# Performance work log

Hardware: AMD Instinct MI355X
Metric: run time of the kernel (lower is better)

The kernel has to match this reference:

```python
import jax, jax.numpy as jnp
import numpy as np

# static module config (matches init_kwargs)
DIM = 128
HEADS = 8
DW, HW, WW = 5, 7, 7  # depth/height/width window


def _neighbor_indices(D, H, W):
    """Flat circular-neighborhood indices, shape (P, n) with P=D*H*W, n=DW*HW*WW."""
    od = np.arange(DW) - (DW - 1) // 2
    oh = np.arange(HW) - (HW - 1) // 2
    ow = np.arange(WW) - (WW - 1) // 2
    dd = (np.arange(D)[:, None] + od[None, :]) % D   # (D, DW)
    hh = (np.arange(H)[:, None] + oh[None, :]) % H   # (H, HW)
    ww = (np.arange(W)[:, None] + ow[None, :]) % W   # (W, WW)
    idx = (dd[:, None, None, :, None, None] * (H * W)
           + hh[None, :, None, None, :, None] * W
           + ww[None, None, :, None, None, :])        # (D,H,W,DW,HW,WW)
    return jnp.asarray(idx.reshape(D * H * W, DW * HW * WW), dtype=jnp.int32)


def setup_inputs() -> dict:
    key = jax.random.key(0)
    k1, k2, k3, k4, k5 = jax.random.split(key, 5)
    B, D, H, W, C = 1, 5, 24, 48, DIM
    w_scale = 1.0 / np.sqrt(C)  # keep attention logits in a sane range
    return {
        "x": jax.random.normal(k1, (B, D, H, W, C), dtype=jnp.float32),
        "qkv_w": jax.random.normal(k2, (3 * C, C), dtype=jnp.float32) * w_scale,
        "qkv_b": jax.random.normal(k3, (3 * C,), dtype=jnp.float32) * 0.01,
        "proj_w": jax.random.normal(k4, (C, C), dtype=jnp.float32) * w_scale,
        "proj_b": jax.random.normal(k5, (C,), dtype=jnp.float32) * 0.01,
    }


def reference(x, qkv_w, qkv_b, proj_w, proj_b):
    B, D, H, W, C = x.shape
    P = D * H * W
    n = DW * HW * WW
    hd = C // HEADS
    scale = hd ** -0.5
    idx = _neighbor_indices(D, H, W)                      # (P, n) int32, static

    xf = x.reshape(B, P, C)
    qkv = xf @ qkv_w.T + qkv_b                            # (B, P, 3C)
    q, k, v = jnp.split(qkv, 3, axis=-1)

    q = q.reshape(B, P, HEADS, hd)                        # center-pixel query
    k_g = k[:, idx].reshape(B, P, n, HEADS, hd)           # gathered circular neighborhood
    v_g = v[:, idx].reshape(B, P, n, HEADS, hd)

    scores = jnp.einsum('bphd,bpnhd->bhpn', q, k_g) * scale
    attn = jax.nn.softmax(scores, axis=-1)                # softmax over 245 neighbors
    out = jnp.einsum('bhpn,bpnhd->bphd', attn, v_g).reshape(B, P, C)
    out = out @ proj_w.T + proj_b
    return out.reshape(B, D, H, W, C)
```

## Files before the change

kernel.cpp:

```cpp
#include <hip/hip_runtime.h>
#include <hip/hip_bf16.h>
#include <cstddef>

#define DIMC   128
#define NHEADS 8
#define HDIM   16
#define DD     5
#define HH     24
#define WW_    48
#define NPOS   (DD * HH * WW_)
#define SCALE  0.25f

typedef short  bf16x8 __attribute__((ext_vector_type(8)));
typedef float  f32x4  __attribute__((ext_vector_type(4)));

__device__ __forceinline__ unsigned short f2bf(float f) {
    unsigned u = __float_as_uint(f);
    u = (u + 0x7FFFu + ((u >> 16) & 1u)) >> 16;
    return (unsigned short)u;
}
__device__ __forceinline__ float bf2f(unsigned short s) {
    return __uint_as_float(((unsigned)s) << 16);
}

__global__ __launch_bounds__(256, 3) void gemm_qkv_kernel(
    const float* __restrict__ x,
    const float* __restrict__ wq,
    const float* __restrict__ qkv_b,
    unsigned short* __restrict__ Qhl,
    unsigned short* __restrict__ Kbf,
    unsigned short* __restrict__ Vbf)
{
    __shared__ __align__(16) unsigned short Bs[64][264];

    const int tid = threadIdx.x;
    const int bn  = blockIdx.x * 64;
    const int bm  = blockIdx.y * 64;

    for (int i = tid; i < 2048; i += 256) {
        const int r = i >> 5, c4 = (i & 31) * 4;
        const float4 v = *(const float4*)(wq + (size_t)(bn + r) * 128 + c4);
        ushort4 hi, lo;
        hi.x = f2bf(v.x); hi.y = f2bf(v.y); hi.z = f2bf(v.z); hi.w = f2bf(v.w);
        lo.x = f2bf(v.x - bf2f(hi.x));
        lo.y = f2bf(v.y - bf2f(hi.y));
        lo.z = f2bf(v.z - bf2f(hi.z));
        lo.w = f2bf(v.w - bf2f(hi.w));
        *(ushort4*)(&Bs[r][c4])       = hi;
        *(ushort4*)(&Bs[r][128 + c4]) = lo;
    }
    __syncthreads();

    const int w    = tid >> 6;
    const int lane = tid & 63;
    const int ln   = lane & 15;
    const int quad = lane >> 4;
    const int row  = bm + w * 16 + ln;
    const float* ar = x + (size_t)row * 128 + quad * 8;

    f32x4 acc[4] = {};
    #pragma unroll
    for (int kcg = 0; kcg < 4; ++kcg) {
        const float4 xa = *(const float4*)(ar + kcg * 32);
        const float4 xb = *(const float4*)(ar + kcg * 32 + 4);
        bf16x8 ahi, alo;
        {
            const float vv[8] = {xa.x, xa.y, xa.z, xa.w, xb.x, xb.y, xb.z, xb.w};
            #pragma unroll
            for (int j = 0; j < 8; ++j) {
                const unsigned short hh = f2bf(vv[j]);
                ahi[j] = (short)hh;
                alo[j] = (short)f2bf(vv[j] - bf2f(hh));
            }
        }
        #pragma unroll
        for (int nt = 0; nt < 4; ++nt) {
            const bf16x8 bhi = *(const bf16x8*)(&Bs[nt * 16 + ln][kcg * 32 + quad * 8]);
            const bf16x8 blo = *(const bf16x8*)(&Bs[nt * 16 + ln][128 + kcg * 32 + quad * 8]);
            acc[nt] = __builtin_amdgcn_mfma_f32_16x16x32_bf16(ahi, bhi, acc[nt], 0, 0, 0);
            acc[nt] = __builtin_amdgcn_mfma_f32_16x16x32_bf16(alo, bhi, acc[nt], 0, 0, 0);
            acc[nt] = __builtin_amdgcn_mfma_f32_16x16x32_bf16(ahi, blo, acc[nt], 0, 0, 0);
        }
    }

    #pragma unroll
    for (int nt = 0; nt < 4; ++nt) {
        const int col = bn + nt * 16 + ln;
        const float bv = qkv_b[col];
        #pragma unroll
        for (int r = 0; r < 4; ++r) {
            const int orow = bm + w * 16 + quad * 4 + r;
            const float val = acc[nt][r] + bv;
            if (col < 128) {
                const int h = col >> 4, ci = col & 15;
                const unsigned short hi = f2bf(val);
                Qhl[(size_t)orow * 256 + h * 32 + ci]      = hi;
                Qhl[(size_t)orow * 256 + h * 32 + 16 + ci] = f2bf(val - bf2f(hi));
            } else if (col < 256) {
                Kbf[(size_t)orow * 128 + (col - 128)] = f2bf(val);
            } else {
                Vbf[(size_t)orow * 128 + (col - 256)] = f2bf(val);
            }
        }
    }
}

__global__ __launch_bounds__(128, 2) void gemm_proj_kernel(
    const float* __restrict__ Opart,
    const float* __restrict__ Lpart,
    const float* __restrict__ wp,
    const float* __restrict__ proj_b,
    float* __restrict__ out)
{
    __shared__ __align__(16) unsigned short Bs[64][264];

    const int tid = threadIdx.x;
    const int bn  = blockIdx.x * 64;
    const int bm  = blockIdx.y * 32;

    for (int i = tid; i < 2048; i += 128) {
        const int r = i >> 5, c4 = (i & 31) * 4;
        const float4 v = *(const float4*)(wp + (size_t)(bn + r) * 128 + c4);
        ushort4 hi, lo;
        hi.x = f2bf(v.x); hi.y = f2bf(v.y); hi.z = f2bf(v.z); hi.w = f2bf(v.w);
        lo.x = f2bf(v.x - bf2f(hi.x));
        lo.y = f2bf(v.y - bf2f(hi.y));
        lo.z = f2bf(v.z - bf2f(hi.z));
        lo.w = f2bf(v.w - bf2f(hi.w));
        *(ushort4*)(&Bs[r][c4])       = hi;
        *(ushort4*)(&Bs[r][128 + c4]) = lo;
    }
    __syncthreads();

    const int w    = tid >> 6;
    const int lane = tid & 63;
    const int ln   = lane & 15;
    const int quad = lane >> 4;
    const int row  = bm + w * 16 + ln;

    float linv[8];
    {
        const float4 l0a = *(const float4*)(Lpart + (size_t)row * 8);
        const float4 l0b = *(const float4*)(Lpart + (size_t)row * 8 + 4);
        const float4 l1a = *(const float4*)(Lpart + (size_t)(NPOS + row) * 8);
        const float4 l1b = *(const float4*)(Lpart + (size_t)(NPOS + row) * 8 + 4);
        linv[0] = 1.0f / (l0a.x + l1a.x); linv[1] = 1.0f / (l0a.y + l1a.y);
        linv[2] = 1.0f / (l0a.z + l1a.z); linv[3] = 1.0f / (l0a.w + l1a.w);
        linv[4] = 1.0f / (l0b.x + l1b.x); linv[5] = 1.0f / (l0b.y + l1b.y);
        linv[6] = 1.0f / (l0b.z + l1b.z); linv[7] = 1.0f / (l0b.w + l1b.w);
    }
    const float* o0 = Opart + (size_t)row * 128 + quad * 8;
    const float* o1 = o0 + (size_t)NPOS * 128;

    f32x4 acc[4] = {};
    #pragma unroll
    for (int kcg = 0; kcg < 4; ++kcg) {
        const float4 a0 = *(const float4*)(o0 + kcg * 32);
        const float4 a0b = *(const float4*)(o0 + kcg * 32 + 4);
        const float4 a1 = *(const float4*)(o1 + kcg * 32);
        const float4 a1b = *(const float4*)(o1 + kcg * 32 + 4);
        const float inv = linv[kcg * 2 + (quad >> 1)];
        const float vv[8] = {
            (a0.x + a1.x) * inv, (a0.y + a1.y) * inv,
            (a0.z + a1.z) * inv, (a0.w + a1.w) * inv,
            (a0b.x + a1b.x) * inv, (a0b.y + a1b.y) * inv,
            (a0b.z + a1b.z) * inv, (a0b.w + a1b.w) * inv };
        bf16x8 ahi, alo;
        #pragma unroll
        for (int j = 0; j < 8; ++j) {
            const unsigned short hh = f2bf(vv[j]);
            ahi[j] = (short)hh;
            alo[j] = (short)f2bf(vv[j] - bf2f(hh));
        }
        #pragma unroll
        for (int nt = 0; nt < 4; ++nt) {
            const bf16x8 bhi = *(const bf16x8*)(&Bs[nt * 16 + ln][kcg * 32 + quad * 8]);
            const bf16x8 blo = *(const bf16x8*)(&Bs[nt * 16 + ln][128 + kcg * 32 + quad * 8]);
            acc[nt] = __builtin_amdgcn_mfma_f32_16x16x32_bf16(ahi, bhi, acc[nt], 0, 0, 0);
            acc[nt] = __builtin_amdgcn_mfma_f32_16x16x32_bf16(alo, bhi, acc[nt], 0, 0, 0);
            acc[nt] = __builtin_amdgcn_mfma_f32_16x16x32_bf16(ahi, blo, acc[nt], 0, 0, 0);
        }
    }

    #pragma unroll
    for (int nt = 0; nt < 4; ++nt) {
        const int col = bn + nt * 16 + ln;
        const float bv = proj_b[col];
        #pragma unroll
        for (int r = 0; r < 4; ++r) {
            const int orow = bm + w * 16 + quad * 4 + r;
            out[(size_t)orow * 128 + col] = acc[nt][r] + bv;
        }
    }
}

__global__ __launch_bounds__(256, 4) void attn_kernel(
    const unsigned short* __restrict__ Qhl,
    const unsigned short* __restrict__ Kbf,
    const unsigned short* __restrict__ Vbf,
    float* __restrict__ Opart,
    float* __restrict__ Lpart)
{
    __shared__ __align__(16) char smem[26368];
    unsigned short (*Vt)[264] = (unsigned short(*)[264])smem;
    unsigned short (*Qb)[40]  = (unsigned short(*)[40])(smem + 8448);
    unsigned short* PwBase    = (unsigned short*)(smem + 14848);
    float* red_l              = (float*)(smem + 25088);
    float* redO               = (float*)smem;

    const int bx   = blockIdx.x;
    const int tile = bx >> 1;
    const int half = bx & 1;
    const int h    = blockIdx.y;
    const int ty0  = (tile / 12) * 4;
    const int tx0  = (tile % 12) * 4;
    const int tid  = threadIdx.x;

    for (int i = tid; i < 512; i += 256) {
        const int ul = i >> 1, hf8 = i & 1;
        const int u  = half * 256 + ul;
        if (u < 500) {
            const int dp = u / 100;
            const int rr = u - dp * 100;
            const int yy = rr / 10;
            const int xx = rr - yy * 10;
            int y = ty0 - 3 + yy; if (y < 0) y += HH;  if (y >= HH) y -= HH;
            int x = tx0 - 3 + xx; if (x < 0) x += WW_; if (x >= WW_) x -= WW_;
            const int g = (dp * HH + y) * WW_ + x;
            const bf16x8 v = *(const bf16x8*)(Vbf + (size_t)g * 128 + h * 16 + hf8 * 8);
            #pragma unroll
            for (int c = 0; c < 8; ++c) Vt[hf8 * 8 + c][ul] = (unsigned short)v[c];
        } else {
            #pragma unroll
            for (int c = 0; c < 8; ++c) Vt[hf8 * 8 + c][ul] = 0;
        }
    }
    for (int i = tid; i < 320; i += 256) {
        const int p = i >> 2, seg = i & 3;
        const int d = p >> 4, s = p & 15;
        const int sy = s >> 2, sx = s & 3;
        const int g = (d * HH + ty0 + sy) * WW_ + tx0 + sx;
        *(bf16x8*)(&Qb[p][seg * 8]) = *(const bf16x8*)(Qhl + (size_t)g * 256 + h * 32 + seg * 8);
    }
    __syncthreads();

    const int w    = tid >> 6;
    const int lane = tid & 63;
    const int ln   = lane & 15;
    const int quad = lane >> 4;
    const int sy   = ln >> 2, sx = ln & 3;

    unsigned short* Pw = PwBase + w * 1280;

    bf16x8 qf[5];
    #pragma unroll
    for (int mt = 0; mt < 5; ++mt)
        qf[mt] = *(const bf16x8*)(&Qb[mt * 16 + ln][quad * 8]);

    f32x4 Ow[5] = {};
    float lsum[5] = {};

    #pragma unroll
    for (int chunk = 0; chunk < 2; ++chunk) {
        const int u0g = (half * 8 + w * 2 + chunk) * 32;
        const int u0l = (w * 2 + chunk) * 32;

        int rowa, rowb;
        {
            const int ua = u0g + ln      < 500 ? u0g + ln      : 499;
            const int ub = u0g + 16 + ln < 500 ? u0g + 16 + ln : 499;
            int dp = ua / 100, rr = ua - dp * 100, yy = rr / 10, xx = rr - yy * 10;
            int y = ty0 - 3 + yy; if (y < 0) y += HH;  if (y >= HH) y -= HH;
            int x = tx0 - 3 + xx; if (x < 0) x += WW_; if (x >= WW_) x -= WW_;
            rowa = (dp * HH + y) * WW_ + x;
            dp = ub / 100; rr = ub - dp * 100; yy = rr / 10; xx = rr - yy * 10;
            y = ty0 - 3 + yy; if (y < 0) y += HH;  if (y >= HH) y -= HH;
            x = tx0 - 3 + xx; if (x < 0) x += WW_; if (x >= WW_) x -= WW_;
            rowb = (dp * HH + y) * WW_ + x;
        }
        const bf16x8 ka = *(const bf16x8*)(Kbf + (size_t)rowa * 128 + h * 16 + (quad & 1) * 8);
        const bf16x8 kb = *(const bf16x8*)(Kbf + (size_t)rowb * 128 + h * 16 + (quad & 1) * 8);

        bool msk[2][4];
        #pragma unroll
        for (int b = 0; b < 2; ++b)
            #pragma unroll
            for (int r = 0; r < 4; ++r) {
                const int u = u0g + 16 * b + 4 * quad + r;
                const int rr = u % 100;
                const int uy = rr / 10, ux = rr - uy * 10;
                msk[b][r] = (u < 500) && ((unsigned)(uy - sy) <= 6u)
                                      && ((unsigned)(ux - sx) <= 6u);
            }

        const bf16x8 vf = *(const bf16x8*)(&Vt[ln][u0l + quad * 8]);

        #pragma unroll
        for (int mt = 0; mt < 5; ++mt) {
            f32x4 s0 = __builtin_amdgcn_mfma_f32_16x16x32_bf16(
                ka, qf[mt], (f32x4){0.f, 0.f, 0.f, 0.f}, 0, 0, 0);
            f32x4 s1 = __builtin_amdgcn_mfma_f32_16x16x32_bf16(
                kb, qf[mt], (f32x4){0.f, 0.f, 0.f, 0.f}, 0, 0, 0);

            unsigned short* pw = Pw + (mt & 1) * 640 + ln * 40;
            #pragma unroll
            for (int b = 0; b < 2; ++b) {
                const f32x4 s = b ? s1 : s0;
                unsigned short e[4];
                #pragma unroll
                for (int r = 0; r < 4; ++r) {
                    const float ev = msk[b][r] ? __expf(fmaf(s[r], SCALE, -8.0f)) : 0.f;
                    e[r] = f2bf(ev);
                    lsum[mt] += bf2f(e[r]);
                }
                *(unsigned*)(pw + 16 * b + 4 * quad)     = (unsigned)e[0] | ((unsigned)e[1] << 16);
                *(unsigned*)(pw + 16 * b + 4 * quad + 2) = (unsigned)e[2] | ((unsigned)e[3] << 16);
            }
            const bf16x8 pf = *(const bf16x8*)(Pw + (mt & 1) * 640 + ln * 40 + quad * 8);
            Ow[mt] = __builtin_amdgcn_mfma_f32_16x16x32_bf16(vf, pf, Ow[mt], 0, 0, 0);
        }
    }

    #pragma unroll
    for (int mt = 0; mt < 5; ++mt) {
        lsum[mt] += __shfl_xor(lsum[mt], 16);
        lsum[mt] += __shfl_xor(lsum[mt], 32);
    }

    __syncthreads();

    if (quad == 0) {
        #pragma unroll
        for (int mt = 0; mt < 5; ++mt)
            red_l[w * 80 + mt * 16 + ln] = lsum[mt];
    }
    #pragma unroll
    for (int mt = 0; mt < 5; ++mt)
        #pragma unroll
        for (int r = 0; r < 4; ++r)
            redO[(size_t)((w * 5 + mt) * 16 + quad * 4 + r) * 16 + ln] = Ow[mt][r];
    __syncthreads();

    for (int i = tid; i < 1280; i += 256) {
        const int m = i >> 4, c = i & 15;
        const int mt = m >> 4, mloc = m & 15;
        float o = 0.f, l = 0.f;
        #pragma unroll
        for (int w4 = 0; w4 < 4; ++w4) {
            o += redO[(size_t)((w4 * 5 + mt) * 16 + c) * 16 + mloc];
            l += red_l[w4 * 80 + m];
        }
        const int qsy = (mloc >> 2), qsx = mloc & 3;
        const size_t g = (size_t)((mt * HH + ty0 + qsy) * WW_ + (tx0 + qsx));
        Opart[((size_t)half * NPOS + g) * 128 + h * HDIM + c] = o;
        if (c == 0) Lpart[((size_t)half * NPOS + g) * 8 + h] = l;
    }
}

extern "C" void kernel_launch(void* const* d_in, const int* in_sizes, int n_in,
                              void* d_out, int out_size, void* d_ws, size_t ws_size,
                              hipStream_t stream)
{
    const float* x      = (const float*)d_in[0];
    const float* qkv_w  = (const float*)d_in[1];
    const float* qkv_b  = (const float*)d_in[2];
    const float* proj_w = (const float*)d_in[3];
    const float* proj_b = (const float*)d_in[4];
    float* out = (float*)d_out;

    char* ws = (char*)d_ws;
    unsigned short* Qhl   = (unsigned short*)ws;  ws += (size_t)NPOS * 256 * 2;
    unsigned short* Kbf   = (unsigned short*)ws;  ws += (size_t)NPOS * 128 * 2;
    unsigned short* Vbf   = (unsigned short*)ws;  ws += (size_t)NPOS * 128 * 2;
    float*          Opart = (float*)ws;           ws += (size_t)2 * NPOS * 128 * 4;
    float*          Lpart = (float*)ws;           ws += (size_t)2 * NPOS * 8 * 4;

    {
        dim3 grid(384 / 64, NPOS / 64);
        gemm_qkv_kernel<<<grid, 256, 0, stream>>>(x, qkv_w, qkv_b, Qhl, Kbf, Vbf);
    }
    {
        dim3 grid(144, NHEADS);
        attn_kernel<<<grid, 256, 0, stream>>>(Qhl, Kbf, Vbf, Opart, Lpart);
    }
    {
        dim3 grid(DIMC / 64, NPOS / 32);
        gemm_proj_kernel<<<grid, 128, 0, stream>>>(Opart, Lpart, proj_w, proj_b, out);
    }
}
```

Measured before the change: 98.86 us.

## Repartition attention work so each wave owns one depth slice, drop cross-wave reduction

The attention kernel now launches 5 waves per block, each handling one depth slice of 16 queries across all 256 keys, instead of 4 waves splitting keys across all 80 queries. This removes the shared-memory reduction of partial outputs and sums and the extra barriers, and lets each wave write its result directly with vector stores. Key row indices and neighbourhood masks are precomputed once into shared memory as an index table and bitmasks. Softmax probabilities are rearranged into the MFMA operand layout with cross-lane shuffles instead of a shared-memory round trip. In exchange, each wave now gathers K for every key chunk itself, which adds redundant global loads across waves.

```diff
diff --git a/kernel.cpp b/kernel.cpp
--- a/kernel.cpp
+++ b/kernel.cpp
@@ -194,19 +194,17 @@
     }
 }
 
-__global__ __launch_bounds__(256, 4) void attn_kernel(
+__global__ __launch_bounds__(320, 4) void attn_kernel(
     const unsigned short* __restrict__ Qhl,
     const unsigned short* __restrict__ Kbf,
     const unsigned short* __restrict__ Vbf,
     float* __restrict__ Opart,
     float* __restrict__ Lpart)
 {
-    __shared__ __align__(16) char smem[26368];
-    unsigned short (*Vt)[264] = (unsigned short(*)[264])smem;
-    unsigned short (*Qb)[40]  = (unsigned short(*)[40])(smem + 8448);
-    unsigned short* PwBase    = (unsigned short*)(smem + 14848);
-    float* red_l              = (float*)(smem + 25088);
-    float* redO               = (float*)smem;
+    __shared__ __align__(16) unsigned short Vt[16][258];
+    __shared__ __align__(16) unsigned short Qb[80][40];
+    __shared__ int RowL[256];
+    __shared__ unsigned short Mb[16][18];
 
     const int bx   = blockIdx.x;
     const int tile = bx >> 1;
@@ -216,16 +214,36 @@
     const int tx0  = (tile % 12) * 4;
     const int tid  = threadIdx.x;
 
-    for (int i = tid; i < 512; i += 256) {
+    for (int ul = tid; ul < 256; ul += 320) {
+        int u = half * 256 + ul; if (u > 499) u = 499;
+        const int dp = u / 100, rr = u % 100;
+        const int uy = rr / 10,  ux = rr % 10;
+        int y = ty0 - 3 + uy; if (y < 0) y += HH;  if (y >= HH) y -= HH;
+        int x = tx0 - 3 + ux; if (x < 0) x += WW_; if (x >= WW_) x -= WW_;
+        RowL[ul] = (dp * HH + y) * WW_ + x;
+    }
+    for (int i = tid; i < 256; i += 320) {
+        const int t = i >> 4, ql = i & 15;
+        const int qsy = ql >> 2, qsx = ql & 3;
+        unsigned bits = 0;
+        #pragma unroll
+        for (int b = 0; b < 16; ++b) {
+            const int u = half * 256 + t * 16 + b;
+            const int rr = u % 100;
+            const int uy = rr / 10, ux = rr % 10;
+            if (u < 500 && (unsigned)(uy - qsy) <= 6u && (unsigned)(ux - qsx) <= 6u)
+                bits |= 1u << b;
+        }
+        Mb[ql][t] = (unsigned short)bits;
+    }
+    for (int i = tid; i < 512; i += 320) {
         const int ul = i >> 1, hf8 = i & 1;
         const int u  = half * 256 + ul;
         if (u < 500) {
-            const int dp = u / 100;
-            const int rr = u - dp * 100;
-            const int yy = rr / 10;
-            const int xx = rr - yy * 10;
-            int y = ty0 - 3 + yy; if (y < 0) y += HH;  if (y >= HH) y -= HH;
-            int x = tx0 - 3 + xx; if (x < 0) x += WW_; if (x >= WW_) x -= WW_;
+            const int dp = u / 100, rr = u % 100;
+            const int uy = rr / 10,  ux = rr % 10;
+            int y = ty0 - 3 + uy; if (y < 0) y += HH;  if (y >= HH) y -= HH;
+            int x = tx0 - 3 + ux; if (x < 0) x += WW_; if (x >= WW_) x -= WW_;
             const int g = (dp * HH + y) * WW_ + x;
             const bf16x8 v = *(const bf16x8*)(Vbf + (size_t)g * 128 + h * 16 + hf8 * 8);
             #pragma unroll
@@ -235,11 +253,11 @@
             for (int c = 0; c < 8; ++c) Vt[hf8 * 8 + c][ul] = 0;
         }
     }
-    for (int i = tid; i < 320; i += 256) {
-        const int p = i >> 2, seg = i & 3;
+    {
+        const int p = tid >> 2, seg = tid & 3;
         const int d = p >> 4, s = p & 15;
-        const int sy = s >> 2, sx = s & 3;
-        const int g = (d * HH + ty0 + sy) * WW_ + tx0 + sx;
+        const int qsy = s >> 2, qsx = s & 3;
+        const int g = (d * HH + ty0 + qsy) * WW_ + tx0 + qsx;
         *(bf16x8*)(&Qb[p][seg * 8]) = *(const bf16x8*)(Qhl + (size_t)g * 256 + h * 32 + seg * 8);
     }
     __syncthreads();
@@ -248,113 +266,73 @@
     const int lane = tid & 63;
     const int ln   = lane & 15;
     const int quad = lane >> 4;
-    const int sy   = ln >> 2, sx = ln & 3;
-
-    unsigned short* Pw = PwBase + w * 1280;
-
-    bf16x8 qf[5];
-    #pragma unroll
-    for (int mt = 0; mt < 5; ++mt)
-        qf[mt] = *(const bf16x8*)(&Qb[mt * 16 + ln][quad * 8]);
-
-    f32x4 Ow[5] = {};
-    float lsum[5] = {};
-
-    #pragma unroll
-    for (int chunk = 0; chunk < 2; ++chunk) {
-        const int u0g = (half * 8 + w * 2 + chunk) * 32;
-        const int u0l = (w * 2 + chunk) * 32;
-
-        int rowa, rowb;
-        {
-            const int ua = u0g + ln      < 500 ? u0g + ln      : 499;
-            const int ub = u0g + 16 + ln < 500 ? u0g + 16 + ln : 499;
-            int dp = ua / 100, rr = ua - dp * 100, yy = rr / 10, xx = rr - yy * 10;
-            int y = ty0 - 3 + yy; if (y < 0) y += HH;  if (y >= HH) y -= HH;
-            int x = tx0 - 3 + xx; if (x < 0) x += WW_; if (x >= WW_) x -= WW_;
-            rowa = (dp * HH + y) * WW_ + x;
-            dp = ub / 100; rr = ub - dp * 100; yy = rr / 10; xx = rr - yy * 10;
-            y = ty0 - 3 + yy; if (y < 0) y += HH;  if (y >= HH) y -= HH;
-            x = tx0 - 3 + xx; if (x < 0) x += WW_; if (x >= WW_) x -= WW_;
-            rowb = (dp * HH + y) * WW_ + x;
-        }
-        const bf16x8 ka = *(const bf16x8*)(Kbf + (size_t)rowa * 128 + h * 16 + (quad & 1) * 8);
-        const bf16x8 kb = *(const bf16x8*)(Kbf + (size_t)rowb * 128 + h * 16 + (quad & 1) * 8);
-
-        bool msk[2][4];
-        #pragma unroll
-        for (int b = 0; b < 2; ++b)
-            #pragma unroll
-            for (int r = 0; r < 4; ++r) {
-                const int u = u0g + 16 * b + 4 * quad + r;
-                const int rr = u % 100;
-                const int uy = rr / 10, ux = rr - uy * 10;
-                msk[b][r] = (u < 500) && ((unsigned)(uy - sy) <= 6u)
-                                      && ((unsigned)(ux - sx) <= 6u);
-            }
+
+    const bf16x8 qf = *(const bf16x8*)(&Qb[w * 16 + ln][quad * 8]);
+    f32x4 Ow = {0.f, 0.f, 0.f, 0.f};
+    float lsum = 0.f;
+
+    const int koff = h * 16 + (quad & 1) * 8;
+    const int qa   = (quad & 1) << 1;
+    const int srcA = ln + (qa << 4);
+    const int srcB = srcA + 16;
+    const bool hi2 = quad >= 2;
+
+    #pragma unroll 2
+    for (int c = 0; c < 8; ++c) {
+        const int u0l = c * 32;
+        const int g0 = RowL[u0l + ln];
+        const int g1 = RowL[u0l + 16 + ln];
+        const bf16x8 ka = *(const bf16x8*)(Kbf + (size_t)g0 * 128 + koff);
+        const bf16x8 kb = *(const bf16x8*)(Kbf + (size_t)g1 * 128 + koff);
+        const unsigned mb = *(const unsigned*)(&Mb[ln][2 * c]);
+        const unsigned m0 = (mb >> (quad * 4)) & 0xF;
+        const unsigned m1 = (mb >> (16 + quad * 4)) & 0xF;
+
+        f32x4 s0 = __builtin_amdgcn_mfma_f32_16x16x32_bf16(ka, qf, (f32x4){0.f,0.f,0.f,0.f}, 0, 0, 0);
+        f32x4 s1 = __builtin_amdgcn_mfma_f32_16x16x32_bf16(kb, qf, (f32x4){0.f,0.f,0.f,0.f}, 0, 0, 0);
+
+        unsigned short e0[4], e1[4];
+        #pragma unroll
+        for (int r = 0; r < 4; ++r) {
+            const float v0 = ((m0 >> r) & 1u) ? __expf(fmaf(s0[r], SCALE, -8.0f)) : 0.f;
+            const float v1 = ((m1 >> r) & 1u) ? __expf(fmaf(s1[r], SCALE, -8.0f)) : 0.f;
+            e0[r] = f2bf(v0);
+            e1[r] = f2bf(v1);
+            lsum += bf2f(e0[r]) + bf2f(e1[r]);
+        }
+        const int dA = (int)((unsigned)e0[0] | ((unsigned)e0[1] << 16));
+        const int dB = (int)((unsigned)e0[2] | ((unsigned)e0[3] << 16));
+        const int dC = (int)((unsigned)e1[0] | ((unsigned)e1[1] << 16));
+        const int dD = (int)((unsigned)e1[2] | ((unsigned)e1[3] << 16));
+
+        const int xA = __shfl(dA, srcA, 64);
+        const int yC = __shfl(dC, srcA, 64);
+        const int xB = __shfl(dB, srcA, 64);
+        const int yD = __shfl(dD, srcA, 64);
+        const int zA = __shfl(dA, srcB, 64);
+        const int wC = __shfl(dC, srcB, 64);
+        const int zB = __shfl(dB, srcB, 64);
+        const int wD = __shfl(dD, srcB, 64);
+
+        union { int u[4]; bf16x8 v; } pf;
+        pf.u[0] = hi2 ? yC : xA;
+        pf.u[1] = hi2 ? yD : xB;
+        pf.u[2] = hi2 ? wC : zA;
+        pf.u[3] = hi2 ? wD : zB;
 
         const bf16x8 vf = *(const bf16x8*)(&Vt[ln][u0l + quad * 8]);
-
-        #pragma unroll
-        for (int mt = 0; mt < 5; ++mt) {
-            f32x4 s0 = __builtin_amdgcn_mfma_f32_16x16x32_bf16(
-                ka, qf[mt], (f32x4){0.f, 0.f, 0.f, 0.f}, 0, 0, 0);
-            f32x4 s1 = __builtin_amdgcn_mfma_f32_16x16x32_bf16(
-                kb, qf[mt], (f32x4){0.f, 0.f, 0.f, 0.f}, 0, 0, 0);
-
-            unsigned short* pw = Pw + (mt & 1) * 640 + ln * 40;
-            #pragma unroll
-            for (int b = 0; b < 2; ++b) {
-                const f32x4 s = b ? s1 : s0;
-                unsigned short e[4];
-                #pragma unroll
-                for (int r = 0; r < 4; ++r) {
-                    const float ev = msk[b][r] ? __expf(fmaf(s[r], SCALE, -8.0f)) : 0.f;
-                    e[r] = f2bf(ev);
-                    lsum[mt] += bf2f(e[r]);
-                }
-                *(unsigned*)(pw + 16 * b + 4 * quad)     = (unsigned)e[0] | ((unsigned)e[1] << 16);
-                *(unsigned*)(pw + 16 * b + 4 * quad + 2) = (unsigned)e[2] | ((unsigned)e[3] << 16);
-            }
-            const bf16x8 pf = *(const bf16x8*)(Pw + (mt & 1) * 640 + ln * 40 + quad * 8);
-            Ow[mt] = __builtin_amdgcn_mfma_f32_16x16x32_bf16(vf, pf, Ow[mt], 0, 0, 0);
-        }
-    }
-
-    #pragma unroll
-    for (int mt = 0; mt < 5; ++mt) {
-        lsum[mt] += __shfl_xor(lsum[mt], 16);
-        lsum[mt] += __shfl_xor(lsum[mt], 32);
-    }
-
-    __syncthreads();
-
-    if (quad == 0) {
-        #pragma unroll
-        for (int mt = 0; mt < 5; ++mt)
-            red_l[w * 80 + mt * 16 + ln] = lsum[mt];
-    }
-    #pragma unroll
-    for (int mt = 0; mt < 5; ++mt)
-        #pragma unroll
-        for (int r = 0; r < 4; ++r)
-            redO[(size_t)((w * 5 + mt) * 16 + quad * 4 + r) * 16 + ln] = Ow[mt][r];
-    __syncthreads();
-
-    for (int i = tid; i < 1280; i += 256) {
-        const int m = i >> 4, c = i & 15;
-        const int mt = m >> 4, mloc = m & 15;
-        float o = 0.f, l = 0.f;
-        #pragma unroll
-        for (int w4 = 0; w4 < 4; ++w4) {
-            o += redO[(size_t)((w4 * 5 + mt) * 16 + c) * 16 + mloc];
-            l += red_l[w4 * 80 + m];
-        }
-        const int qsy = (mloc >> 2), qsx = mloc & 3;
-        const size_t g = (size_t)((mt * HH + ty0 + qsy) * WW_ + (tx0 + qsx));
-        Opart[((size_t)half * NPOS + g) * 128 + h * HDIM + c] = o;
-        if (c == 0) Lpart[((size_t)half * NPOS + g) * 8 + h] = l;
-    }
+        Ow = __builtin_amdgcn_mfma_f32_16x16x32_bf16(vf, pf.v, Ow, 0, 0, 0);
+    }
+
+    lsum += __shfl_xor(lsum, 16);
+    lsum += __shfl_xor(lsum, 32);
+
+    const int qsy = ln >> 2, qsx = ln & 3;
+    const size_t g = (size_t)((w * HH + ty0 + qsy) * WW_ + (tx0 + qsx));
+    *(float4*)(Opart + ((size_t)half * NPOS + g) * 128 + h * 16 + quad * 4) =
+        make_float4(Ow[0], Ow[1], Ow[2], Ow[3]);
+    if (quad == 0)
+        Lpart[((size_t)half * NPOS + g) * 8 + h] = lsum;
 }
 
 extern "C" void kernel_launch(void* const* d_in, const int* in_sizes, int n_in,
@@ -381,7 +359,7 @@
     }
     {
         dim3 grid(144, NHEADS);
-        attn_kernel<<<grid, 256, 0, stream>>>(Qhl, Kbf, Vbf, Opart, Lpart);
+        attn_kernel<<<grid, 320, 0, stream>>>(Qhl, Kbf, Vbf, Opart, Lpart);
     }
     {
         dim3 grid(DIMC / 64, NPOS / 32);
```

After: 101.1 us. +2.3%, slower.

## Interleave K and V per head in a head-major layout for attention gathers

Applied to the files above, without the earlier changes.

The QKV GEMM now writes K and V into a single head-major buffer where each position holds 16 K values followed by 16 V values for that head. The attention kernel gathers neighbour K and V from this compact 64-byte-per-row layout instead of strided 256-byte rows of separate K and V arrays, which should improve cache-line use and locality for the scattered neighbourhood loads. It also shrinks the shared-memory V-transpose row pitch from 264 to 258, which changes the LDS bank pattern. The GEMM epilogue stores become more scattered in exchange.

```diff
diff --git a/kernel.cpp b/kernel.cpp
--- a/kernel.cpp
+++ b/kernel.cpp
@@ -28,8 +28,7 @@
     const float* __restrict__ wq,
     const float* __restrict__ qkv_b,
     unsigned short* __restrict__ Qhl,
-    unsigned short* __restrict__ Kbf,
-    unsigned short* __restrict__ Vbf)
+    unsigned short* __restrict__ KV)
 {
     __shared__ __align__(16) unsigned short Bs[64][264];
 
@@ -97,9 +96,11 @@
                 Qhl[(size_t)orow * 256 + h * 32 + ci]      = hi;
                 Qhl[(size_t)orow * 256 + h * 32 + 16 + ci] = f2bf(val - bf2f(hi));
             } else if (col < 256) {
-                Kbf[(size_t)orow * 128 + (col - 128)] = f2bf(val);
+                const int h = (col - 128) >> 4, ci = (col - 128) & 15;
+                KV[((size_t)h * NPOS + orow) * 32 + ci] = f2bf(val);
             } else {
-                Vbf[(size_t)orow * 128 + (col - 256)] = f2bf(val);
+                const int h = (col - 256) >> 4, ci = (col - 256) & 15;
+                KV[((size_t)h * NPOS + orow) * 32 + 16 + ci] = f2bf(val);
             }
         }
     }
@@ -196,13 +197,12 @@
 
 __global__ __launch_bounds__(256, 4) void attn_kernel(
     const unsigned short* __restrict__ Qhl,
-    const unsigned short* __restrict__ Kbf,
-    const unsigned short* __restrict__ Vbf,
+    const unsigned short* __restrict__ KV,
     float* __restrict__ Opart,
     float* __restrict__ Lpart)
 {
     __shared__ __align__(16) char smem[26368];
-    unsigned short (*Vt)[264] = (unsigned short(*)[264])smem;
+    unsigned short (*Vt)[258] = (unsigned short(*)[258])smem;
     unsigned short (*Qb)[40]  = (unsigned short(*)[40])(smem + 8448);
     unsigned short* PwBase    = (unsigned short*)(smem + 14848);
     float* red_l              = (float*)(smem + 25088);
@@ -216,18 +216,18 @@
     const int tx0  = (tile % 12) * 4;
     const int tid  = threadIdx.x;
 
+    const unsigned short* KVh = KV + (size_t)h * NPOS * 32;
+
     for (int i = tid; i < 512; i += 256) {
         const int ul = i >> 1, hf8 = i & 1;
         const int u  = half * 256 + ul;
         if (u < 500) {
-            const int dp = u / 100;
-            const int rr = u - dp * 100;
-            const int yy = rr / 10;
-            const int xx = rr - yy * 10;
-            int y = ty0 - 3 + yy; if (y < 0) y += HH;  if (y >= HH) y -= HH;
-            int x = tx0 - 3 + xx; if (x < 0) x += WW_; if (x >= WW_) x -= WW_;
+            const int dp = u / 100, rr = u % 100;
+            const int uy = rr / 10, ux = rr % 10;
+            int y = ty0 - 3 + uy; if (y < 0) y += HH;  if (y >= HH) y -= HH;
+            int x = tx0 - 3 + ux; if (x < 0) x += WW_; if (x >= WW_) x -= WW_;
             const int g = (dp * HH + y) * WW_ + x;
-            const bf16x8 v = *(const bf16x8*)(Vbf + (size_t)g * 128 + h * 16 + hf8 * 8);
+            const bf16x8 v = *(const bf16x8*)(KVh + (size_t)g * 32 + 16 + hf8 * 8);
             #pragma unroll
             for (int c = 0; c < 8; ++c) Vt[hf8 * 8 + c][ul] = (unsigned short)v[c];
         } else {
@@ -278,8 +278,8 @@
             x = tx0 - 3 + xx; if (x < 0) x += WW_; if (x >= WW_) x -= WW_;
             rowb = (dp * HH + y) * WW_ + x;
         }
-        const bf16x8 ka = *(const bf16x8*)(Kbf + (size_t)rowa * 128 + h * 16 + (quad & 1) * 8);
-        const bf16x8 kb = *(const bf16x8*)(Kbf + (size_t)rowb * 128 + h * 16 + (quad & 1) * 8);
+        const bf16x8 ka = *(const bf16x8*)(KVh + (size_t)rowa * 32 + (quad & 1) * 8);
+        const bf16x8 kb = *(const bf16x8*)(KVh + (size_t)rowb * 32 + (quad & 1) * 8);
 
         bool msk[2][4];
         #pragma unroll
@@ -370,18 +370,17 @@
 
     char* ws = (char*)d_ws;
     unsigned short* Qhl   = (unsigned short*)ws;  ws += (size_t)NPOS * 256 * 2;
-    unsigned short* Kbf   = (unsigned short*)ws;  ws += (size_t)NPOS * 128 * 2;
-    unsigned short* Vbf   = (unsigned short*)ws;  ws += (size_t)NPOS * 128 * 2;
+    unsigned short* KV    = (unsigned short*)ws;  ws += (size_t)NHEADS * NPOS * 32 * 2;
     float*          Opart = (float*)ws;           ws += (size_t)2 * NPOS * 128 * 4;
     float*          Lpart = (float*)ws;           ws += (size_t)2 * NPOS * 8 * 4;
 
     {
         dim3 grid(384 / 64, NPOS / 64);
-        gemm_qkv_kernel<<<grid, 256, 0, stream>>>(x, qkv_w, qkv_b, Qhl, Kbf, Vbf);
+        gemm_qkv_kernel<<<grid, 256, 0, stream>>>(x, qkv_w, qkv_b, Qhl, KV);
     }
     {
         dim3 grid(144, NHEADS);
-        attn_kernel<<<grid, 256, 0, stream>>>(Qhl, Kbf, Vbf, Opart, Lpart);
+        attn_kernel<<<grid, 256, 0, stream>>>(Qhl, KV, Opart, Lpart);
     }
     {
         dim3 grid(DIMC / 64, NPOS / 32);
```

Measured after the change: 99.83 us. Within noise of the previous version (+1.0%).
